# Performance work log

Measured on AMD Instinct MI355X. Metric: run time of the kernel, lower is better.

The kernel has to match this reference:

```python
import jax, jax.numpy as jnp
import numpy as np

R = 0.2          # stable-distribution hash bucket width
TABLE_SIZE = 2   # hash table size (buckets)
M = 5            # number of appended ALSH transform dims
EPS = 1e-12


def conv2d(x, W, b, pad):
    out = jax.lax.conv_general_dilated(
        x, W, window_strides=(1, 1), padding=[(pad, pad), (pad, pad)],
        dimension_numbers=('NCHW', 'OIHW', 'NCHW'))
    return out + b[None, :, None, None]


def maxpool2(x):
    return jax.lax.reduce_window(x, -jnp.inf, jax.lax.max,
                                 (1, 1, 2, 2), (1, 1, 2, 2), 'VALID')


def alsh_mask(x, W, a, c):
    """ALSH filter selection: hash P(kernels) and Q(query) with a stable
    distribution hash h(v)=floor((a.v+b)/r) mod table_size; active filters
    are those landing in the query's bucket. Returns [B, Cout] 0/1 mask.
    Multiplying conv output by this mask == gather active filters then
    zero_fill_missing back to full channel count."""
    Cout, Cin, kH, kW = W.shape
    Kf = W.reshape(Cout, -1)                       # [Cout, Cin*kH*kW]
    norms = jnp.linalg.norm(Kf, axis=1)
    Kn = Kf / (jnp.max(norms) + EPS)               # scale so all norms <= 1
    n = jnp.linalg.norm(Kn, axis=1, keepdims=True)
    # P transform: append norm^2, norm^4, ..., norm^(2^M)
    powers = jnp.concatenate([n ** (2 ** (i + 1)) for i in range(M)], axis=1)
    P = jnp.concatenate([Kn, powers], axis=1)      # [Cout, d+M]
    kh = jnp.mod(jnp.floor((P @ a + c[0]) / R), TABLE_SIZE)  # [Cout]
    # query vector: per-sample channel means broadcast over kernel support
    cm = x.mean(axis=(2, 3))                       # [B, Cin]
    q = jnp.repeat(cm, kH * kW, axis=1)            # [B, Cin*kH*kW] (cin,kh,kw order)
    qn = q / (jnp.linalg.norm(q, axis=1, keepdims=True) + EPS)
    # Q transform: append M halves
    Qv = jnp.concatenate([qn, jnp.full((q.shape[0], M), 0.5, q.dtype)], axis=1)
    qh = jnp.mod(jnp.floor((Qv @ a + c[0]) / R), TABLE_SIZE)  # [B]
    return (kh[None, :] == qh[:, None]).astype(x.dtype)       # [B, Cout]


def setup_inputs() -> dict:
    key = jax.random.key(0)
    ks = jax.random.split(key, 16)
    u = lambda k, s: jax.random.uniform(k, s, jnp.float32, 0.0, R)
    n = lambda k, s, sc=0.1: jax.random.normal(k, s, jnp.float32) * sc
    return {
        'x': jax.random.normal(ks[0], (4096, 3, 32, 32), jnp.float32),
        'W1': n(ks[1], (16, 3, 5, 5)), 'b1': n(ks[2], (16,)),
        'a1': jax.random.normal(ks[3], (80,), jnp.float32), 'c1': u(ks[4], (1,)),
        'W2': n(ks[5], (20, 16, 5, 5)), 'b2': n(ks[6], (20,)),
        'a2': jax.random.normal(ks[7], (405,), jnp.float32), 'c2': u(ks[8], (1,)),
        'W3': n(ks[9], (20, 20, 5, 5)), 'b3': n(ks[10], (20,)),
        'a3': jax.random.normal(ks[11], (505,), jnp.float32), 'c3': u(ks[12], (1,)),
        'Wo': n(ks[13], (10, 320)), 'bo': n(ks[14], (10,)),
    }


def reference(x, W1, b1, a1, c1, W2, b2, a2, c2, W3, b3, a3, c3, Wo, bo):
    m1 = alsh_mask(x, W1, a1, c1)
    h = jax.nn.relu(conv2d(x, W1, b1, 2)) * m1[:, :, None, None]
    h = maxpool2(h)                                # [B,16,16,16]
    m2 = alsh_mask(h, W2, a2, c2)
    h = jax.nn.relu(conv2d(h, W2, b2, 2)) * m2[:, :, None, None]
    h = maxpool2(h)                                # [B,20,8,8]
    m3 = alsh_mask(h, W3, a3, c3)
    h = jax.nn.relu(conv2d(h, W3, b3, 2)) * m3[:, :, None, None]
    # zero_fill_missing -> identity here: inactive channels already zero
    h = maxpool2(h)                                # [B,20,4,4]
    flat = h.reshape(h.shape[0], -1)               # [B,320]
    return flat @ Wo.T + bo
```

## Files before the change

### kernel.cpp

```cpp
#include <hip/hip_runtime.h>
#include <hip/hip_bf16.h>

#define EPSV 1e-12
#define RHASH 0.2

__device__ __forceinline__ int fmod2(double t) {
    return (int)(((long long)floor(t)) & 1LL);
}

__device__ __forceinline__ void load_row6(const float* base, float* r) {
    float2 a0 = *(const float2*)(base);
    float2 a1 = *(const float2*)(base + 2);
    float2 a2 = *(const float2*)(base + 4);
    r[0] = a0.x; r[1] = a0.y; r[2] = a1.x; r[3] = a1.y; r[4] = a2.x; r[5] = a2.y;
}

__device__ __forceinline__ void load_row12(const float* base, float* r) {
    #pragma unroll
    for (int j = 0; j < 6; ++j) *(float2*)&r[2 * j] = *(const float2*)(base + 2 * j);
}

#define FMA4(c,kx,w) { float wg=(w); \
  acc[c][0]=fmaf(wg,cur[kx],acc[c][0]); acc[c][1]=fmaf(wg,cur[(kx)+1],acc[c][1]); \
  acc[c][2]=fmaf(wg,nxt[kx],acc[c][2]); acc[c][3]=fmaf(wg,nxt[(kx)+1],acc[c][3]); }

__device__ void layer_setup(const float* W, const float* a, double cval,
                            int Co, int Ci, int* kh, double* asum, double* qc,
                            double* s_norm, float* Wbuf, float* abuf)
{
    const int t = threadIdx.x;
    const int D = Ci * 25;
    for (int i = t; i < Co * D; i += 256) Wbuf[i] = W[i];
    for (int i = t; i < D + 5; i += 256) abuf[i] = a[i];
    __syncthreads();
    if (t < Co) {
        double s = 0;
        for (int j = 0; j < D; ++j) { double w = (double)Wbuf[t * D + j]; s += w * w; }
        s_norm[t] = sqrt(s);
    }
    __syncthreads();
    if (t == 0) {
        double mx = 0;
        for (int i = 0; i < Co; ++i) mx = fmax(mx, s_norm[i]);
        s_norm[23] = 1.0 / (mx + EPSV);
    }
    __syncthreads();
    double scale = s_norm[23];
    if (t < Co) {
        double dp = 0;
        for (int j = 0; j < D; ++j) dp += (double)Wbuf[t * D + j] * (double)abuf[j];
        dp *= scale;
        double n = s_norm[t] * scale;
        double p = n * n;
        for (int m = 0; m < 5; ++m) { dp += p * (double)abuf[D + m]; p *= p; }
        kh[t] = fmod2((dp + cval) / RHASH);
    }
    if (t >= 64 && t < 64 + Ci) {
        int c = t - 64;
        double s = 0;
        for (int j = 0; j < 25; ++j) s += (double)abuf[c * 25 + j];
        asum[c] = s;
    }
    if (t == 128) {
        double s = 0;
        for (int m = 0; m < 5; ++m) s += (double)abuf[D + m];
        *qc = 0.5 * s + cval;
    }
    __syncthreads();
}

__global__ __launch_bounds__(256) void setup_kernel(
    const float* W1, const float* a1, const float* c1,
    const float* W2, const float* a2, const float* c2,
    const float* W3, const float* a3, const float* c3,
    double* dmeta, int* imeta)
{
    __shared__ float Wbuf[10000];
    __shared__ float abuf[512];
    __shared__ double s_norm[24];
    layer_setup(W1, a1, (double)c1[0], 16, 3,  imeta + 0,  dmeta + 0,  dmeta + 39, s_norm, Wbuf, abuf);
    layer_setup(W2, a2, (double)c2[0], 20, 16, imeta + 16, dmeta + 3,  dmeta + 40, s_norm, Wbuf, abuf);
    layer_setup(W3, a3, (double)c3[0], 20, 20, imeta + 36, dmeta + 19, dmeta + 41, s_norm, Wbuf, abuf);
}

__global__ __launch_bounds__(256) void pack_kernel(const float* W1, const float* W2, const float* W3,
                                                   float* Wp1, float* Wp2, float* Wp3)
{
    int i = blockIdx.x * 256 + threadIdx.x;
    if (i < 1200) {
        int co = i & 15, r = i >> 4;
        int kx = r % 5, r2 = r / 5, ky = r2 % 5, ci = r2 / 5;
        Wp1[i] = W1[co * 75 + ci * 25 + ky * 5 + kx];
    } else if (i < 1200 + 8960) {
        int k = i - 1200;
        int j = k % 28, r = k / 28;
        int cog = r % 4, r2 = r / 4, ky = r2 % 5, ci = r2 / 5;
        Wp2[k] = (j < 25) ? W2[(cog * 5 + j / 5) * 400 + ci * 25 + ky * 5 + (j % 5)] : 0.f;
    } else if (i < 1200 + 8960 + 11200) {
        int k = i - 10160;
        int j = k % 28, r = k / 28;
        int cog = r % 4, r2 = r / 4, ky = r2 % 5, ci = r2 / 5;
        Wp3[k] = (j < 25) ? W3[(cog * 5 + j / 5) * 500 + ci * 25 + ky * 5 + (j % 5)] : 0.f;
    }
}

__global__ __launch_bounds__(256) void conv1_kernel(
    const float* __restrict__ x, const float* __restrict__ Wp1,
    const float* __restrict__ b1, const int* __restrict__ kh1,
    const double* __restrict__ dmeta, float* __restrict__ h1,
    int* __restrict__ qh2)
{
    __shared__ float xs[3][36][38];
    __shared__ float Ws[1200];
    __shared__ double s_red[3];
    __shared__ double s_ch[16][4];

    const int b = blockIdx.x, t = threadIdx.x;
    const int w = t >> 6, ln = t & 63;

    for (int i = t; i < 3 * 36 * 38; i += 256) (&xs[0][0][0])[i] = 0.f;
    for (int i = t; i < 600; i += 256) ((float2*)Ws)[i] = ((const float2*)Wp1)[i];
    __syncthreads();
    const float2* xb2 = (const float2*)(x + (size_t)b * 3072);
    for (int i = t; i < 1536; i += 256) {
        int c = i >> 9, rem = i & 511;
        int row = rem >> 4, col2 = rem & 15;
        *(float2*)&xs[c][row + 2][col2 * 2 + 2] = xb2[i];
    }
    __syncthreads();

    if (w < 3) {
        double s = 0;
        for (int j = 0; j < 16; ++j) {
            int i = ln + 64 * j;
            s += (double)xs[w][(i >> 5) + 2][(i & 31) + 2];
        }
        #pragma unroll
        for (int off = 32; off; off >>= 1) s += __shfl_xor(s, off);
        if (ln == 0) s_red[w] = s;
    }
    __syncthreads();
    double dp = 0, nn = 0;
    #pragma unroll
    for (int c = 0; c < 3; ++c) {
        double cm = s_red[c] * (1.0 / 1024.0);
        dp += cm * dmeta[c]; nn += cm * cm;
    }
    const int qh = fmod2((dp / (5.0 * sqrt(nn) + EPSV) + dmeta[39]) / RHASH);

    const int cog = ln >> 4;
    const int py = 4 * w + ((ln >> 2) & 3), pxg = ln & 3;
    const int y0 = 2 * py, x0 = 8 * pxg;

    float accA[4][8], accB[4][8];
    #pragma unroll
    for (int c = 0; c < 4; ++c) {
        float bb = b1[cog * 4 + c];
        #pragma unroll
        for (int k = 0; k < 8; ++k) { accA[c][k] = bb; accB[c][k] = bb; }
    }

    #pragma unroll
    for (int ci = 0; ci < 3; ++ci) {
        float ra[12], rb[12];
        load_row12(&xs[ci][y0][x0],     ra);
        load_row12(&xs[ci][y0 + 1][x0], rb);
        #pragma unroll
        for (int ky = 0; ky < 5; ++ky) {
            const float4* wq = (const float4*)&Ws[((ci * 5 + ky) * 5) * 16 + cog * 4];
            #pragma unroll
            for (int kx = 0; kx < 5; ++kx) {
                float4 wv = wq[kx * 4];
                { float wg = wv.x;
                  #pragma unroll
                  for (int k = 0; k < 8; ++k) { accA[0][k] = fmaf(wg, ra[k + kx], accA[0][k]);
                                                accB[0][k] = fmaf(wg, rb[k + kx], accB[0][k]); } }
                { float wg = wv.y;
                  #pragma unroll
                  for (int k = 0; k < 8; ++k) { accA[1][k] = fmaf(wg, ra[k + kx], accA[1][k]);
                                                accB[1][k] = fmaf(wg, rb[k + kx], accB[1][k]); } }
                { float wg = wv.z;
                  #pragma unroll
                  for (int k = 0; k < 8; ++k) { accA[2][k] = fmaf(wg, ra[k + kx], accA[2][k]);
                                                accB[2][k] = fmaf(wg, rb[k + kx], accB[2][k]); } }
                { float wg = wv.w;
                  #pragma unroll
                  for (int k = 0; k < 8; ++k) { accA[3][k] = fmaf(wg, ra[k + kx], accA[3][k]);
                                                accB[3][k] = fmaf(wg, rb[k + kx], accB[3][k]); } }
            }
            if (ky < 4) {
                #pragma unroll
                for (int j = 0; j < 12; ++j) ra[j] = rb[j];
                load_row12(&xs[ci][y0 + ky + 2][x0], rb);
            }
        }
    }

    float* hb = h1 + (size_t)b * 4096 + py * 16 + pxg * 4;
    double csum[4];
    #pragma unroll
    for (int c = 0; c < 4; ++c) {
        int co = cog * 4 + c;
        float mask = (kh1[co] == qh) ? 1.f : 0.f;
        float v0 = fmaxf(fmaxf(accA[c][0], accA[c][1]), fmaxf(accB[c][0], accB[c][1]));
        float v1 = fmaxf(fmaxf(accA[c][2], accA[c][3]), fmaxf(accB[c][2], accB[c][3]));
        float v2 = fmaxf(fmaxf(accA[c][4], accA[c][5]), fmaxf(accB[c][4], accB[c][5]));
        float v3 = fmaxf(fmaxf(accA[c][6], accA[c][7]), fmaxf(accB[c][6], accB[c][7]));
        v0 = fmaxf(v0, 0.f) * mask; v1 = fmaxf(v1, 0.f) * mask;
        v2 = fmaxf(v2, 0.f) * mask; v3 = fmaxf(v3, 0.f) * mask;
        *(float4*)(hb + co * 256) = make_float4(v0, v1, v2, v3);
        csum[c] = (double)v0 + (double)v1 + (double)v2 + (double)v3;
    }
    #pragma unroll
    for (int c = 0; c < 4; ++c) {
        double s = csum[c];
        s += __shfl_xor(s, 8); s += __shfl_xor(s, 4);
        s += __shfl_xor(s, 2); s += __shfl_xor(s, 1);
        if ((ln & 15) == 0) s_ch[cog * 4 + c][w] = s;
    }
    __syncthreads();
    if (t == 0) {
        double dp2 = 0, nn2 = 0;
        #pragma unroll
        for (int c = 0; c < 16; ++c) {
            double cm = (s_ch[c][0] + s_ch[c][1] + s_ch[c][2] + s_ch[c][3]) * (1.0 / 256.0);
            dp2 += cm * dmeta[3 + c]; nn2 += cm * cm;
        }
        qh2[b] = fmod2((dp2 / (5.0 * sqrt(nn2) + EPSV) + dmeta[40]) / RHASH);
    }
}

__global__ __launch_bounds__(256) void conv2_kernel(
    const float* __restrict__ h1, const float* __restrict__ Wp2,
    const float* __restrict__ b2, const int* __restrict__ kh2,
    const int* __restrict__ qh2, const double* __restrict__ dmeta,
    float* __restrict__ h2, int* __restrict__ qh3, int B)
{
    __shared__ float xs[4][4][20][22];
    __shared__ float Ws[2240];
    __shared__ double s_ch[4][20];

    const int b0 = blockIdx.x * 4, t = threadIdx.x;
    const int s = t >> 6, l = t & 63;
    const int cog = l >> 4, pos = l & 15;
    const int py = pos >> 1, pxg = pos & 1;
    const int b = b0 + s;

    for (int i = t; i < 4 * 4 * 20 * 22; i += 256) (&xs[0][0][0][0])[i] = 0.f;

    const int qh = (b < B) ? qh2[b] : 0;
    float accA[5][8], accB[5][8];
    #pragma unroll
    for (int c = 0; c < 5; ++c) {
        float bb = b2[cog * 5 + c];
        #pragma unroll
        for (int k = 0; k < 8; ++k) { accA[c][k] = bb; accB[c][k] = bb; }
    }
    __syncthreads();

    for (int ch = 0; ch < 4; ++ch) {
        for (int i = t; i < 1120; i += 256)
            ((float2*)Ws)[i] = ((const float2*)(Wp2 + ch * 2240))[i];
        for (int i = t; i < 2048; i += 256) {
            int si = i >> 9, rem = i & 511, cil = rem >> 7, rr = rem & 127;
            int p2 = rr * 2, row = p2 >> 4, col = p2 & 15;
            if (b0 + si < B)
                *(float2*)&xs[si][cil][row + 2][col + 2] =
                    ((const float2*)(h1 + (size_t)(b0 + si) * 4096 + (size_t)(ch * 4 + cil) * 256))[rr];
        }
        __syncthreads();

        for (int cil = 0; cil < 4; ++cil) {
            float ra[12], rb[12];
            load_row12(&xs[s][cil][2 * py][8 * pxg],     ra);
            load_row12(&xs[s][cil][2 * py + 1][8 * pxg], rb);
            #pragma unroll
            for (int ky = 0; ky < 5; ++ky) {
                float wv[28];
                const float4* wp = (const float4*)&Ws[((cil * 5 + ky) * 4 + cog) * 28];
                *(float4*)&wv[0]  = wp[0];
                *(float4*)&wv[4]  = wp[1];
                *(float4*)&wv[8]  = wp[2];
                *(float4*)&wv[12] = wp[3];
                *(float4*)&wv[16] = wp[4];
                *(float4*)&wv[20] = wp[5];
                *(float4*)&wv[24] = wp[6];
                #pragma unroll
                for (int c = 0; c < 5; ++c) {
                    #pragma unroll
                    for (int kx = 0; kx < 5; ++kx) {
                        float wg = wv[c * 5 + kx];
                        #pragma unroll
                        for (int k = 0; k < 8; ++k) {
                            accA[c][k] = fmaf(wg, ra[k + kx], accA[c][k]);
                            accB[c][k] = fmaf(wg, rb[k + kx], accB[c][k]);
                        }
                    }
                }
                if (ky < 4) {
                    #pragma unroll
                    for (int j = 0; j < 12; ++j) ra[j] = rb[j];
                    load_row12(&xs[s][cil][2 * py + ky + 2][8 * pxg], rb);
                }
            }
        }
        __syncthreads();
    }

    float* ob = h2 + (size_t)b * 1280 + py * 8 + pxg * 4;
    double csum[5];
    #pragma unroll
    for (int c = 0; c < 5; ++c) {
        int co = cog * 5 + c;
        float mask = (kh2[co] == qh) ? 1.f : 0.f;
        float v0 = fmaxf(fmaxf(accA[c][0], accA[c][1]), fmaxf(accB[c][0], accB[c][1]));
        float v1 = fmaxf(fmaxf(accA[c][2], accA[c][3]), fmaxf(accB[c][2], accB[c][3]));
        float v2 = fmaxf(fmaxf(accA[c][4], accA[c][5]), fmaxf(accB[c][4], accB[c][5]));
        float v3 = fmaxf(fmaxf(accA[c][6], accA[c][7]), fmaxf(accB[c][6], accB[c][7]));
        v0 = fmaxf(v0, 0.f) * mask; v1 = fmaxf(v1, 0.f) * mask;
        v2 = fmaxf(v2, 0.f) * mask; v3 = fmaxf(v3, 0.f) * mask;
        if (b < B) *(float4*)(ob + co * 64) = make_float4(v0, v1, v2, v3);
        csum[c] = (double)v0 + (double)v1 + (double)v2 + (double)v3;
    }
    #pragma unroll
    for (int c = 0; c < 5; ++c) {
        double sv = csum[c];
        sv += __shfl_xor(sv, 8); sv += __shfl_xor(sv, 4);
        sv += __shfl_xor(sv, 2); sv += __shfl_xor(sv, 1);
        if (pos == 0) s_ch[s][cog * 5 + c] = sv;
    }
    __syncthreads();
    if (l == 0 && b < B) {
        double dp2 = 0, nn2 = 0;
        #pragma unroll
        for (int c = 0; c < 20; ++c) {
            double cm = s_ch[s][c] * (1.0 / 64.0);
            dp2 += cm * dmeta[19 + c]; nn2 += cm * cm;
        }
        qh3[b] = fmod2((dp2 / (5.0 * sqrt(nn2) + EPSV) + dmeta[41]) / RHASH);
    }
}

__global__ __launch_bounds__(256) void conv3_kernel(
    const float* __restrict__ h2, const float* __restrict__ Wp3,
    const float* __restrict__ b3, const int* __restrict__ kh3,
    const int* __restrict__ qh3,
    const float* __restrict__ Wo, const float* __restrict__ bo,
    float* __restrict__ out, int B)
{
    __shared__ float xs[4][5][12][12];
    __shared__ float Ws[2800];
    __shared__ float flat[4][320];

    const int b0 = blockIdx.x * 4, t = threadIdx.x;
    const int s = t >> 6, q0 = t & 63, cog = q0 >> 4, pos = q0 & 15;
    const int py = pos >> 2, px = pos & 3;
    const int y0 = 2 * py, x0 = 2 * px;
    const int b = b0 + s;

    for (int i = t; i < 4 * 5 * 144; i += 256) (&xs[0][0][0][0])[i] = 0.f;

    const int qh = (b < B) ? qh3[b] : 0;
    float acc[5][4];
    #pragma unroll
    for (int c = 0; c < 5; ++c) {
        float bb = b3[cog * 5 + c];
        acc[c][0] = bb; acc[c][1] = bb; acc[c][2] = bb; acc[c][3] = bb;
    }
    __syncthreads();

    for (int ch = 0; ch < 4; ++ch) {
        for (int i = t; i < 1400; i += 256)
            ((float2*)Ws)[i] = ((const float2*)(Wp3 + ch * 2800))[i];
        for (int i = t; i < 640; i += 256) {
            int ss = i / 160, r = i - ss * 160, ci = r >> 5, rr = r & 31, p2 = rr * 2;
            if (b0 + ss < B)
                *(float2*)&xs[ss][ci][(p2 >> 3) + 2][(p2 & 7) + 2] =
                    ((const float2*)(h2 + (size_t)(b0 + ss) * 1280 + (ch * 5 + ci) * 64))[rr];
        }
        __syncthreads();

        #pragma unroll
        for (int ci = 0; ci < 5; ++ci) {
            float cur[6], nxt[6];
            load_row6(&xs[s][ci][y0][x0], cur);
            load_row6(&xs[s][ci][y0 + 1][x0], nxt);
            #pragma unroll
            for (int ky = 0; ky < 5; ++ky) {
                const float* wrow = &Ws[((ci * 5 + ky) * 4 + cog) * 28];
                const float4* wq = (const float4*)wrow;
                float4 q;
                q = wq[0]; FMA4(0, 0, q.x) FMA4(0, 1, q.y) FMA4(0, 2, q.z) FMA4(0, 3, q.w)
                q = wq[1]; FMA4(0, 4, q.x) FMA4(1, 0, q.y) FMA4(1, 1, q.z) FMA4(1, 2, q.w)
                q = wq[2]; FMA4(1, 3, q.x) FMA4(1, 4, q.y) FMA4(2, 0, q.z) FMA4(2, 1, q.w)
                q = wq[3]; FMA4(2, 2, q.x) FMA4(2, 3, q.y) FMA4(2, 4, q.z) FMA4(3, 0, q.w)
                q = wq[4]; FMA4(3, 1, q.x) FMA4(3, 2, q.y) FMA4(3, 3, q.z) FMA4(3, 4, q.w)
                q = wq[5]; FMA4(4, 0, q.x) FMA4(4, 1, q.y) FMA4(4, 2, q.z) FMA4(4, 3, q.w)
                FMA4(4, 4, wrow[24])
                if (ky < 4) {
                    #pragma unroll
                    for (int j = 0; j < 6; ++j) cur[j] = nxt[j];
                    load_row6(&xs[s][ci][y0 + ky + 2][x0], nxt);
                }
            }
        }
        __syncthreads();
    }

    #pragma unroll
    for (int c = 0; c < 5; ++c) {
        int co = cog * 5 + c;
        float m = fmaxf(fmaxf(acc[c][0], acc[c][1]), fmaxf(acc[c][2], acc[c][3]));
        flat[s][co * 16 + pos] = fmaxf(m, 0.f) * ((kh3[co] == qh) ? 1.f : 0.f);
    }
    __syncthreads();

    if (t < 160) {
        const int g = t >> 2, qq = t & 3;
        const int ss = g / 10, o = g - ss * 10;
        float a = 0.f;
        const float* wr = Wo + o * 320;
        for (int k = qq; k < 320; k += 4) a = fmaf(flat[ss][k], wr[k], a);
        a += __shfl_xor(a, 1);
        a += __shfl_xor(a, 2);
        if (qq == 0 && b0 + ss < B) out[(size_t)(b0 + ss) * 10 + o] = a + bo[o];
    }
}

extern "C" void kernel_launch(void* const* d_in, const int* in_sizes, int n_in,
                              void* d_out, int out_size, void* d_ws, size_t ws_size,
                              hipStream_t stream)
{
    const float* x  = (const float*)d_in[0];
    const float* W1 = (const float*)d_in[1];
    const float* b1 = (const float*)d_in[2];
    const float* a1 = (const float*)d_in[3];
    const float* c1 = (const float*)d_in[4];
    const float* W2 = (const float*)d_in[5];
    const float* b2 = (const float*)d_in[6];
    const float* a2 = (const float*)d_in[7];
    const float* c2 = (const float*)d_in[8];
    const float* W3 = (const float*)d_in[9];
    const float* b3 = (const float*)d_in[10];
    const float* a3 = (const float*)d_in[11];
    const float* c3 = (const float*)d_in[12];
    const float* Wo = (const float*)d_in[13];
    const float* bo = (const float*)d_in[14];
    float* out = (float*)d_out;

    const int B = in_sizes[0] / 3072;

    float* h1  = (float*)d_ws;
    float* h2  = h1 + (size_t)B * 4096;
    float* Wp1 = h2 + (size_t)B * 1280;
    float* Wp2 = Wp1 + 1200;
    float* Wp3 = Wp2 + 8960;
    double* dmeta = (double*)(Wp3 + 11200);
    int* imeta = (int*)(dmeta + 42);
    int* qh2 = imeta + 56;
    int* qh3 = qh2 + B;

    setup_kernel<<<1, 256, 0, stream>>>(W1, a1, c1, W2, a2, c2, W3, a3, c3, dmeta, imeta);
    pack_kernel<<<84, 256, 0, stream>>>(W1, W2, W3, Wp1, Wp2, Wp3);
    conv1_kernel<<<B, 256, 0, stream>>>(x, Wp1, b1, imeta, dmeta, h1, qh2);
    conv2_kernel<<<(B + 3) / 4, 256, 0, stream>>>(h1, Wp2, b2, imeta + 16, qh2, dmeta, h2, qh3, B);
    conv3_kernel<<<(B + 3) / 4, 256, 0, stream>>>(h2, Wp3, b3, imeta + 36, qh3, Wo, bo, out, B);
}
```

Measured before the change: 514.0 us.

## Merge setup and pack kernels; register-prefetch next chunk in conv2/conv3

Folds the single-block setup kernel and the weight pack kernel into one launch, with blocks 0-2 each handling one layer's hash setup in parallel instead of one block doing all three in sequence. In conv2 and conv3, the next input-channel chunk of activations (and weights in conv3) is loaded into registers while the current chunk is being computed, then written to shared memory. This hides global load latency behind the FMA loop and saves one launch. The cost is higher register pressure, which could lower occupancy.

```diff
diff --git a/kernel.cpp b/kernel.cpp
--- a/kernel.cpp
+++ b/kernel.cpp
@@ -69,38 +69,40 @@
     __syncthreads();
 }
 
-__global__ __launch_bounds__(256) void setup_kernel(
+__global__ __launch_bounds__(256) void prep_kernel(
     const float* W1, const float* a1, const float* c1,
     const float* W2, const float* a2, const float* c2,
     const float* W3, const float* a3, const float* c3,
-    double* dmeta, int* imeta)
+    double* dmeta, int* imeta,
+    float* Wp1, float* Wp2, float* Wp3)
 {
     __shared__ float Wbuf[10000];
     __shared__ float abuf[512];
     __shared__ double s_norm[24];
-    layer_setup(W1, a1, (double)c1[0], 16, 3,  imeta + 0,  dmeta + 0,  dmeta + 39, s_norm, Wbuf, abuf);
-    layer_setup(W2, a2, (double)c2[0], 20, 16, imeta + 16, dmeta + 3,  dmeta + 40, s_norm, Wbuf, abuf);
-    layer_setup(W3, a3, (double)c3[0], 20, 20, imeta + 36, dmeta + 19, dmeta + 41, s_norm, Wbuf, abuf);
-}
-
-__global__ __launch_bounds__(256) void pack_kernel(const float* W1, const float* W2, const float* W3,
-                                                   float* Wp1, float* Wp2, float* Wp3)
-{
-    int i = blockIdx.x * 256 + threadIdx.x;
-    if (i < 1200) {
-        int co = i & 15, r = i >> 4;
-        int kx = r % 5, r2 = r / 5, ky = r2 % 5, ci = r2 / 5;
-        Wp1[i] = W1[co * 75 + ci * 25 + ky * 5 + kx];
-    } else if (i < 1200 + 8960) {
-        int k = i - 1200;
-        int j = k % 28, r = k / 28;
-        int cog = r % 4, r2 = r / 4, ky = r2 % 5, ci = r2 / 5;
-        Wp2[k] = (j < 25) ? W2[(cog * 5 + j / 5) * 400 + ci * 25 + ky * 5 + (j % 5)] : 0.f;
-    } else if (i < 1200 + 8960 + 11200) {
-        int k = i - 10160;
-        int j = k % 28, r = k / 28;
-        int cog = r % 4, r2 = r / 4, ky = r2 % 5, ci = r2 / 5;
-        Wp3[k] = (j < 25) ? W3[(cog * 5 + j / 5) * 500 + ci * 25 + ky * 5 + (j % 5)] : 0.f;
+    const int blk = blockIdx.x;
+    if (blk == 0) {
+        layer_setup(W1, a1, (double)c1[0], 16, 3,  imeta + 0,  dmeta + 0,  dmeta + 39, s_norm, Wbuf, abuf);
+    } else if (blk == 1) {
+        layer_setup(W2, a2, (double)c2[0], 20, 16, imeta + 16, dmeta + 3,  dmeta + 40, s_norm, Wbuf, abuf);
+    } else if (blk == 2) {
+        layer_setup(W3, a3, (double)c3[0], 20, 20, imeta + 36, dmeta + 19, dmeta + 41, s_norm, Wbuf, abuf);
+    } else {
+        int i = (blk - 3) * 256 + threadIdx.x;
+        if (i < 1200) {
+            int co = i & 15, r = i >> 4;
+            int kx = r % 5, r2 = r / 5, ky = r2 % 5, ci = r2 / 5;
+            Wp1[i] = W1[co * 75 + ci * 25 + ky * 5 + kx];
+        } else if (i < 1200 + 8960) {
+            int k = i - 1200;
+            int j = k % 28, r = k / 28;
+            int cog = r % 4, r2 = r / 4, ky = r2 % 5, ci = r2 / 5;
+            Wp2[k] = (j < 25) ? W2[(cog * 5 + j / 5) * 400 + ci * 25 + ky * 5 + (j % 5)] : 0.f;
+        } else if (i < 1200 + 8960 + 11200) {
+            int k = i - 10160;
+            int j = k % 28, r = k / 28;
+            int cog = r % 4, r2 = r / 4, ky = r2 % 5, ci = r2 / 5;
+            Wp3[k] = (j < 25) ? W3[(cog * 5 + j / 5) * 500 + ci * 25 + ky * 5 + (j % 5)] : 0.f;
+        }
     }
 }
 
@@ -230,6 +232,22 @@
     }
 }
 
+#define C2_XLOAD(CH, RX) { \
+    _Pragma("unroll") \
+    for (int j = 0; j < 8; ++j) { \
+        int i = t + 256 * j, si = i >> 9, rem = i & 511, cil = rem >> 7, rr = rem & 127; \
+        RX[j] = (b0 + si < B) ? ((const float2*)h1)[(size_t)(b0 + si) * 2048 + ((CH) * 4 + cil) * 128 + rr] \
+                              : make_float2(0.f, 0.f); \
+    } }
+
+#define C2_XCOMMIT(RX) { \
+    _Pragma("unroll") \
+    for (int j = 0; j < 8; ++j) { \
+        int i = t + 256 * j, si = i >> 9, rem = i & 511, cil = rem >> 7, rr = rem & 127; \
+        int p2 = rr * 2, row = p2 >> 4, col = p2 & 15; \
+        *(float2*)&xs[si][cil][row + 2][col + 2] = RX[j]; \
+    } }
+
 __global__ __launch_bounds__(256) void conv2_kernel(
     const float* __restrict__ h1, const float* __restrict__ Wp2,
     const float* __restrict__ b2, const int* __restrict__ kh2,
@@ -256,19 +274,16 @@
         #pragma unroll
         for (int k = 0; k < 8; ++k) { accA[c][k] = bb; accB[c][k] = bb; }
     }
-    __syncthreads();
+
+    float2 rx[8];
+    C2_XLOAD(0, rx);
 
     for (int ch = 0; ch < 4; ++ch) {
         for (int i = t; i < 1120; i += 256)
             ((float2*)Ws)[i] = ((const float2*)(Wp2 + ch * 2240))[i];
-        for (int i = t; i < 2048; i += 256) {
-            int si = i >> 9, rem = i & 511, cil = rem >> 7, rr = rem & 127;
-            int p2 = rr * 2, row = p2 >> 4, col = p2 & 15;
-            if (b0 + si < B)
-                *(float2*)&xs[si][cil][row + 2][col + 2] =
-                    ((const float2*)(h1 + (size_t)(b0 + si) * 4096 + (size_t)(ch * 4 + cil) * 256))[rr];
-        }
+        C2_XCOMMIT(rx);
         __syncthreads();
+        if (ch < 3) C2_XLOAD(ch + 1, rx);
 
         for (int cil = 0; cil < 4; ++cil) {
             float ra[12], rb[12];
@@ -341,6 +356,41 @@
     }
 }
 
+#define C3_WLOAD(CH, RW) { \
+    _Pragma("unroll") \
+    for (int j = 0; j < 6; ++j) { \
+        int i = t + 256 * j; \
+        if (i < 1400) RW[j] = ((const float2*)(Wp3 + (CH) * 2800))[i]; \
+    } }
+
+#define C3_WCOMMIT(RW) { \
+    _Pragma("unroll") \
+    for (int j = 0; j < 6; ++j) { \
+        int i = t + 256 * j; \
+        if (i < 1400) ((float2*)Ws)[i] = RW[j]; \
+    } }
+
+#define C3_XLOAD(CH, RX) { \
+    _Pragma("unroll") \
+    for (int j = 0; j < 3; ++j) { \
+        int i = t + 256 * j; \
+        if (i < 640) { \
+            int ss = i / 160, r = i - ss * 160, ci = r >> 5, rr = r & 31; \
+            RX[j] = (b0 + ss < B) ? ((const float2*)(h2 + (size_t)(b0 + ss) * 1280 + ((CH) * 5 + ci) * 64))[rr] \
+                                  : make_float2(0.f, 0.f); \
+        } \
+    } }
+
+#define C3_XCOMMIT(RX) { \
+    _Pragma("unroll") \
+    for (int j = 0; j < 3; ++j) { \
+        int i = t + 256 * j; \
+        if (i < 640) { \
+            int ss = i / 160, r = i - ss * 160, ci = r >> 5, rr = r & 31, p2 = rr * 2; \
+            *(float2*)&xs[ss][ci][(p2 >> 3) + 2][(p2 & 7) + 2] = RX[j]; \
+        } \
+    } }
+
 __global__ __launch_bounds__(256) void conv3_kernel(
     const float* __restrict__ h2, const float* __restrict__ Wp3,
     const float* __restrict__ b3, const int* __restrict__ kh3,
@@ -367,18 +417,16 @@
         float bb = b3[cog * 5 + c];
         acc[c][0] = bb; acc[c][1] = bb; acc[c][2] = bb; acc[c][3] = bb;
     }
-    __syncthreads();
+
+    float2 rw[6], rx[3];
+    C3_WLOAD(0, rw);
+    C3_XLOAD(0, rx);
 
     for (int ch = 0; ch < 4; ++ch) {
-        for (int i = t; i < 1400; i += 256)
-            ((float2*)Ws)[i] = ((const float2*)(Wp3 + ch * 2800))[i];
-        for (int i = t; i < 640; i += 256) {
-            int ss = i / 160, r = i - ss * 160, ci = r >> 5, rr = r & 31, p2 = rr * 2;
-            if (b0 + ss < B)
-                *(float2*)&xs[ss][ci][(p2 >> 3) + 2][(p2 & 7) + 2] =
-                    ((const float2*)(h2 + (size_t)(b0 + ss) * 1280 + (ch * 5 + ci) * 64))[rr];
-        }
+        C3_WCOMMIT(rw);
+        C3_XCOMMIT(rx);
         __syncthreads();
+        if (ch < 3) { C3_WLOAD(ch + 1, rw); C3_XLOAD(ch + 1, rx); }
 
         #pragma unroll
         for (int ci = 0; ci < 5; ++ci) {
@@ -460,8 +508,8 @@
     int* qh2 = imeta + 56;
     int* qh3 = qh2 + B;
 
-    setup_kernel<<<1, 256, 0, stream>>>(W1, a1, c1, W2, a2, c2, W3, a3, c3, dmeta, imeta);
-    pack_kernel<<<84, 256, 0, stream>>>(W1, W2, W3, Wp1, Wp2, Wp3);
+    prep_kernel<<<87, 256, 0, stream>>>(W1, a1, c1, W2, a2, c2, W3, a3, c3,
+                                        dmeta, imeta, Wp1, Wp2, Wp3);
     conv1_kernel<<<B, 256, 0, stream>>>(x, Wp1, b1, imeta, dmeta, h1, qh2);
     conv2_kernel<<<(B + 3) / 4, 256, 0, stream>>>(h1, Wp2, b2, imeta + 16, qh2, dmeta, h2, qh3, B);
     conv3_kernel<<<(B + 3) / 4, 256, 0, stream>>>(h2, Wp3, b3, imeta + 36, qh3, Wo, bo, out, B);
```

Result: faster. 487.3 us (-5.2%).
